# Performance work log

Measured on AMD Instinct MI355X. Metric: run time of the kernel, lower is better.

The kernel has to match this reference:

```python
import jax, jax.numpy as jnp
import numpy as np
from jax import lax

N, H, W, C = 4, 256, 256, 128
COUT = 128
BS_IN, BS_OUT, BSTR = 18, 16, 16  # gather block, conv-out block, block stride
N_ACTIVE = 512


def setup_inputs() -> dict:
    key = jax.random.key(0)
    ks = jax.random.split(key, 8)
    x = jax.random.normal(ks[0], (N, H, W, C), dtype=jnp.float32)
    w = jax.random.normal(ks[1], (3, 3, C, COUT), dtype=jnp.float32) * 0.05  # HWIO
    b = jax.random.normal(ks[2], (COUT,), dtype=jnp.float32) * 0.05
    gamma = jax.random.uniform(ks[3], (COUT,), dtype=jnp.float32, minval=0.5, maxval=1.5)
    beta = jax.random.normal(ks[4], (COUT,), dtype=jnp.float32) * 0.1
    mean = jax.random.normal(ks[5], (COUT,), dtype=jnp.float32) * 0.1
    var = jax.random.uniform(ks[6], (COUT,), dtype=jnp.float32, minval=0.5, maxval=1.5)
    # unique active block ids over the N x (H/16) x (W/16) grid -> disjoint scatter targets
    n_blocks = N * (H // BSTR) * (W // BSTR)
    active = jax.random.permutation(ks[7], n_blocks)[:N_ACTIVE].astype(jnp.int32)
    return {"x": x, "w": w, "b": b, "gamma": gamma, "beta": beta,
            "mean": mean, "var": var, "active": active}


def reference(x, w, b, gamma, beta, mean, var, active):
    n_, h_, w_, c_ = x.shape
    nby, nbx = h_ // BSTR, w_ // BSTR
    bn = active // (nby * nbx)
    rem = active % (nby * nbx)
    by = rem // nbx
    bx = rem % nbx

    # --- sparse_gather: overlapping BS_IN x BS_IN input blocks (zero-pad edges) ---
    pad = BS_IN - BS_OUT
    xp = jnp.pad(x, ((0, 0), (0, pad), (0, pad), (0, 0)))
    Hp, Wp = h_ + pad, w_ + pad
    d_in = jnp.arange(BS_IN, dtype=jnp.int32)
    hs = by[:, None] * BSTR + d_in[None, :]            # [Nb, 18]
    ws = bx[:, None] * BSTR + d_in[None, :]            # [Nb, 18]
    gidx = bn[:, None, None] * (Hp * Wp) + hs[:, :, None] * Wp + ws[:, None, :]
    p = xp.reshape(-1, c_)[gidx]                       # [Nb, 18, 18, C]

    # --- dense conv + BN(eval, eps=1e-3) + ReLU on gathered blocks ---
    q = lax.conv_general_dilated(p, w, window_strides=(1, 1), padding='VALID',
                                 dimension_numbers=('NHWC', 'HWIO', 'NHWC'))
    q = q + b
    q = (q - mean) * (gamma * lax.rsqrt(var + 1e-3)) + beta
    q = jax.nn.relu(q)                                 # [Nb, 16, 16, COUT]

    # --- sparse_scatter: write disjoint BS_OUT blocks back into a copy of x ---
    d_out = jnp.arange(BS_OUT, dtype=jnp.int32)
    hso = by[:, None] * BSTR + d_out[None, :]
    wso = bx[:, None] * BSTR + d_out[None, :]
    sidx = bn[:, None, None] * (h_ * w_) + hso[:, :, None] * w_ + wso[:, None, :]
    y = x.reshape(-1, c_).at[sidx.reshape(-1)].set(q.reshape(-1, q.shape[-1]))
    return y.reshape(n_, h_, w_, c_)
```

## Files before the change

### kernel.cpp

```cpp
#include <hip/hip_runtime.h>
#include <hip/hip_bf16.h>

#define H_ 256
#define W_ 256
#define C_ 128
#define NBPOS 1024
#define NACT 512

typedef __bf16 bf16x8 __attribute__((ext_vector_type(8)));
typedef float f32x4 __attribute__((ext_vector_type(4)));

#define SCALE_OFF 294912
#define SHIFT_OFF 295424
#define FLAGS_OFF 295936

__global__ void prep_w_kernel(const float* __restrict__ w, __bf16* __restrict__ wprep) {
  int o = blockIdx.x * 256 + threadIdx.x;
  int j = o & 7, cout = (o >> 3) & 127, k8 = (o >> 10) & 15, tap = o >> 14;
  wprep[o] = (__bf16)w[((size_t)tap * 128 + k8 * 8 + j) * 128 + cout];
}

__global__ void small_kernel(const float* __restrict__ b, const float* __restrict__ gamma,
                             const float* __restrict__ beta, const float* __restrict__ mean,
                             const float* __restrict__ var, const int* __restrict__ active,
                             float* __restrict__ scale, float* __restrict__ shift,
                             int* __restrict__ flags) {
  __shared__ unsigned mask[32];
  int tid = threadIdx.x;
  if (tid < 32) mask[tid] = 0u;
  __syncthreads();
  if (tid < NACT) {
    int a = active[tid];
    atomicOr(&mask[a >> 5], 1u << (a & 31));
  }
  if (tid < 128) {
    float s = gamma[tid] * rsqrtf(var[tid] + 1e-3f);
    scale[tid] = s;
    shift[tid] = (b[tid] - mean[tid]) * s + beta[tid];
  }
  __syncthreads();
  flags[tid] = (mask[tid >> 5] >> (tid & 31)) & 1u;
}

__global__ __launch_bounds__(256) void copy_kernel(const float* __restrict__ x,
                                                   const int* __restrict__ flags,
                                                   float* __restrict__ y) {
  int pb = blockIdx.x;
  if (flags[pb]) return;
  int bn = pb >> 8, by = (pb >> 4) & 15, bx = pb & 15;
  size_t base4 = ((((size_t)bn * H_ + by * 16) * W_ + bx * 16) * C_) >> 2;
  const f32x4* __restrict__ xs = (const f32x4*)x;
  f32x4* __restrict__ ys = (f32x4*)y;
#pragma unroll 4
  for (int i = 0; i < 32; ++i) {
    int lin = (i << 8) + threadIdx.x;
    int row = lin >> 9, rem = lin & 511;
    size_t idx4 = base4 + (size_t)row * (W_ * C_ / 4) + rem;
    f32x4 v = xs[idx4];
    __builtin_nontemporal_store(v, &ys[idx4]);
  }
}

__global__ __launch_bounds__(256, 4) void conv_kernel(
    const float* __restrict__ x, const __bf16* __restrict__ wprep,
    const float* __restrict__ scale, const float* __restrict__ shift,
    const int* __restrict__ active, float* __restrict__ y) {
  __shared__ unsigned char ldsA[180 * 128];
  __shared__ unsigned char ldsB[2][8192];

  const int tid = threadIdx.x;
  const int lane = tid & 63;
  const int wid = tid >> 6;
  const int aid = active[blockIdx.x >> 1];
  const int mh = blockIdx.x & 1;
  const int bn = aid >> 8, by = (aid >> 4) & 15, bx = aid & 15;
  const int h0 = by * 16, w0 = bx * 16;
  const int hm = h0 + mh * 8;
  const float* xb = x + (size_t)bn * (H_ * W_ * C_);

  f32x4 acc[2][8];
  f32x4 zero = {0.f, 0.f, 0.f, 0.f};
#pragma unroll
  for (int i = 0; i < 2; ++i)
#pragma unroll
    for (int j = 0; j < 8; ++j) acc[i][j] = zero;

  const uint4* wp4 = (const uint4*)wprep;
  uint4 t0, t1;
  auto load_t = [&](int u) {
    int ks = u % 18, h = u / 18;
    int tile = ((ks >> 1) << 2) + (h << 1) + (ks & 1);
    t0 = wp4[tile * 512 + tid];
    t1 = wp4[tile * 512 + 256 + tid];
  };
  auto stage = [&](int half) {
    for (int u = tid; u < 180 * 8; u += 256) {
      int s = u >> 3, c8 = u & 7;
      int pr = s / 18, col = s - pr * 18;
      int hs = hm + pr, wsp = w0 + col;
      float4 f0 = make_float4(0.f, 0.f, 0.f, 0.f), f1 = f0;
      if (hs < H_ && wsp < W_) {
        const float* p = xb + (size_t)(hs * W_ + wsp) * C_ + half * 64 + c8 * 8;
        f0 = *(const float4*)p;
        f1 = *(const float4*)(p + 4);
      }
      bf16x8 v;
      v[0] = (__bf16)f0.x; v[1] = (__bf16)f0.y; v[2] = (__bf16)f0.z; v[3] = (__bf16)f0.w;
      v[4] = (__bf16)f1.x; v[5] = (__bf16)f1.y; v[6] = (__bf16)f1.z; v[7] = (__bf16)f1.w;
      int lin = s * 128 + c8 * 16;
      *(bf16x8*)(&ldsA[lin ^ ((s & 7) << 4)]) = v;
    }
  };

  load_t(0);
  stage(0);
  ((uint4*)ldsB[0])[tid] = t0;
  ((uint4*)ldsB[0])[256 + tid] = t1;
  load_t(1);
  __syncthreads();

  const int koff = (lane >> 4) * 16;
  const int colb = (lane & 15) * 16;
  const int krow = (lane >> 4) * 2048;

  for (int u = 0; u < 36; ++u) {
    int cur = u & 1;
    if (u < 35) {
      ((uint4*)ldsB[cur ^ 1])[tid] = t0;
      ((uint4*)ldsB[cur ^ 1])[256 + tid] = t1;
      if (u < 34) load_t(u + 2);
    }
    int ks = u % 18;
    int tap = ks >> 1, kch = ks & 1;
    int dyv = tap / 3, dxv = tap - dyv * 3;

    bf16x8 a[2];
#pragma unroll
    for (int mi = 0; mi < 2; ++mi) {
      int srow = (wid * 2 + mi + dyv) * 18 + dxv + (lane & 15);
      int lin = srow * 128 + kch * 64 + koff;
      a[mi] = *(const bf16x8*)(&ldsA[lin ^ ((srow & 7) << 4)]);
    }
    bf16x8 bfr[8];
#pragma unroll
    for (int nb = 0; nb < 8; ++nb)
      bfr[nb] = *(const bf16x8*)(&ldsB[cur][krow + nb * 256 + colb]);
#pragma unroll
    for (int mi = 0; mi < 2; ++mi)
#pragma unroll
      for (int nb = 0; nb < 8; ++nb)
        acc[mi][nb] = __builtin_amdgcn_mfma_f32_16x16x32_bf16(a[mi], bfr[nb], acc[mi][nb], 0, 0, 0);

    __syncthreads();
    if (u == 17) {
      stage(1);
      __syncthreads();
    }
  }

  const int colc = lane & 15;
  float sc[8], sh[8];
#pragma unroll
  for (int nb = 0; nb < 8; ++nb) {
    sc[nb] = scale[nb * 16 + colc];
    sh[nb] = shift[nb * 16 + colc];
  }
  float* yb = y + (((size_t)bn * H_ + hm) * W_ + w0) * C_;
#pragma unroll
  for (int mi = 0; mi < 2; ++mi) {
    int oy = wid * 2 + mi;
#pragma unroll
    for (int r = 0; r < 4; ++r) {
      int ox = (lane >> 4) * 4 + r;
      float* yr = yb + ((size_t)oy * W_ + ox) * C_;
#pragma unroll
      for (int nb = 0; nb < 8; ++nb) {
        float v = acc[mi][nb][r] * sc[nb] + sh[nb];
        __builtin_nontemporal_store(fmaxf(v, 0.f), &yr[nb * 16 + colc]);
      }
    }
  }
}

extern "C" void kernel_launch(void* const* d_in, const int* in_sizes, int n_in,
                              void* d_out, int out_size, void* d_ws, size_t ws_size,
                              hipStream_t stream) {
  const float* x     = (const float*)d_in[0];
  const float* w     = (const float*)d_in[1];
  const float* b     = (const float*)d_in[2];
  const float* gamma = (const float*)d_in[3];
  const float* beta  = (const float*)d_in[4];
  const float* mean  = (const float*)d_in[5];
  const float* var   = (const float*)d_in[6];
  const int*   act   = (const int*)d_in[7];
  float* y = (float*)d_out;
  char* ws = (char*)d_ws;
  __bf16* wprep = (__bf16*)ws;
  float* scale = (float*)(ws + SCALE_OFF);
  float* shift = (float*)(ws + SHIFT_OFF);
  int* flags = (int*)(ws + FLAGS_OFF);

  prep_w_kernel<<<dim3(576), dim3(256), 0, stream>>>(w, wprep);
  small_kernel<<<dim3(1), dim3(1024), 0, stream>>>(b, gamma, beta, mean, var, act,
                                                   scale, shift, flags);
  copy_kernel<<<dim3(NBPOS), dim3(256), 0, stream>>>(x, flags, y);
  conv_kernel<<<dim3(NACT * 2), dim3(256), 0, stream>>>(x, wprep, scale, shift, act, y);
}
```

Baseline: 79.70 us.

## Merge prep kernels and interleave copy blocks with conv blocks in one launch

Folds the weight-prep and BN/flag kernels into one launch and compacts inactive block ids into a list, so no copy blocks are launched only to exit early. The copy of the inactive blocks is merged into the conv kernel, with every third workgroup doing a copy, so memory-bound copying overlaps with MFMA-bound conv work. This cuts two launches and the idle early-exit workgroups. In exchange the copy workgroups carry the conv kernel's LDS footprint and launch bounds, which may limit how many fit per CU.

Result: faster. 75.26 us (-5.6%).

```diff
diff --git a/kernel.cpp b/kernel.cpp
--- a/kernel.cpp
+++ b/kernel.cpp
@@ -12,25 +12,28 @@
 
 #define SCALE_OFF 294912
 #define SHIFT_OFF 295424
-#define FLAGS_OFF 295936
-
-__global__ void prep_w_kernel(const float* __restrict__ w, __bf16* __restrict__ wprep) {
-  int o = blockIdx.x * 256 + threadIdx.x;
-  int j = o & 7, cout = (o >> 3) & 127, k8 = (o >> 10) & 15, tap = o >> 14;
-  wprep[o] = (__bf16)w[((size_t)tap * 128 + k8 * 8 + j) * 128 + cout];
-}
-
-__global__ void small_kernel(const float* __restrict__ b, const float* __restrict__ gamma,
-                             const float* __restrict__ beta, const float* __restrict__ mean,
-                             const float* __restrict__ var, const int* __restrict__ active,
-                             float* __restrict__ scale, float* __restrict__ shift,
-                             int* __restrict__ flags) {
+#define INACT_OFF 295936
+
+__global__ void prep_kernel(const float* __restrict__ w, const float* __restrict__ b,
+                            const float* __restrict__ gamma, const float* __restrict__ beta,
+                            const float* __restrict__ mean, const float* __restrict__ var,
+                            const int* __restrict__ active,
+                            __bf16* __restrict__ wprep, float* __restrict__ scale,
+                            float* __restrict__ shift, int* __restrict__ inact) {
+  int blk = blockIdx.x, tid = threadIdx.x;
+  if (blk < 576) {
+    int o = blk * 256 + tid;
+    int j = o & 7, cout = (o >> 3) & 127, k8 = (o >> 10) & 15, tap = o >> 14;
+    wprep[o] = (__bf16)w[((size_t)tap * 128 + k8 * 8 + j) * 128 + cout];
+    return;
+  }
   __shared__ unsigned mask[32];
-  int tid = threadIdx.x;
+  __shared__ int cnt;
   if (tid < 32) mask[tid] = 0u;
+  if (tid == 0) cnt = 0;
   __syncthreads();
-  if (tid < NACT) {
-    int a = active[tid];
+  for (int i = tid; i < NACT; i += 256) {
+    int a = active[i];
     atomicOr(&mask[a >> 5], 1u << (a & 31));
   }
   if (tid < 128) {
@@ -39,40 +42,47 @@
     shift[tid] = (b[tid] - mean[tid]) * s + beta[tid];
   }
   __syncthreads();
-  flags[tid] = (mask[tid >> 5] >> (tid & 31)) & 1u;
+  for (int p = tid; p < NBPOS; p += 256) {
+    if (!((mask[p >> 5] >> (p & 31)) & 1u)) {
+      int q = atomicAdd(&cnt, 1);
+      inact[q] = p;
+    }
+  }
 }
 
-__global__ __launch_bounds__(256) void copy_kernel(const float* __restrict__ x,
-                                                   const int* __restrict__ flags,
-                                                   float* __restrict__ y) {
-  int pb = blockIdx.x;
-  if (flags[pb]) return;
-  int bn = pb >> 8, by = (pb >> 4) & 15, bx = pb & 15;
-  size_t base4 = ((((size_t)bn * H_ + by * 16) * W_ + bx * 16) * C_) >> 2;
-  const f32x4* __restrict__ xs = (const f32x4*)x;
-  f32x4* __restrict__ ys = (f32x4*)y;
-#pragma unroll 4
-  for (int i = 0; i < 32; ++i) {
-    int lin = (i << 8) + threadIdx.x;
-    int row = lin >> 9, rem = lin & 511;
-    size_t idx4 = base4 + (size_t)row * (W_ * C_ / 4) + rem;
-    f32x4 v = xs[idx4];
-    __builtin_nontemporal_store(v, &ys[idx4]);
-  }
-}
-
-__global__ __launch_bounds__(256, 4) void conv_kernel(
+__global__ __launch_bounds__(256, 4) void main_kernel(
     const float* __restrict__ x, const __bf16* __restrict__ wprep,
     const float* __restrict__ scale, const float* __restrict__ shift,
-    const int* __restrict__ active, float* __restrict__ y) {
+    const int* __restrict__ active, const int* __restrict__ inact,
+    float* __restrict__ y) {
   __shared__ unsigned char ldsA[180 * 128];
   __shared__ unsigned char ldsB[2][8192];
 
+  const int idx = blockIdx.x;
   const int tid = threadIdx.x;
+
+  if (idx % 3 == 2) {
+    const int cid = inact[idx / 3];
+    const int cn = cid >> 8, cy = (cid >> 4) & 15, cx = cid & 15;
+    const size_t base4 = ((((size_t)cn * H_ + cy * 16) * W_ + cx * 16) * C_) >> 2;
+    const f32x4* __restrict__ xs = (const f32x4*)x;
+    f32x4* __restrict__ ys = (f32x4*)y;
+#pragma unroll 4
+    for (int i = 0; i < 32; ++i) {
+      int lin = (i << 8) + tid;
+      int row = lin >> 9, rem = lin & 511;
+      size_t idx4 = base4 + (size_t)row * (W_ * C_ / 4) + rem;
+      f32x4 v = xs[idx4];
+      __builtin_nontemporal_store(v, &ys[idx4]);
+    }
+    return;
+  }
+
+  const int j = (idx / 3) * 2 + (idx % 3);
   const int lane = tid & 63;
   const int wid = tid >> 6;
-  const int aid = active[blockIdx.x >> 1];
-  const int mh = blockIdx.x & 1;
+  const int aid = active[j >> 1];
+  const int mh = j & 1;
   const int bn = aid >> 8, by = (aid >> 4) & 15, bx = aid & 15;
   const int h0 = by * 16, w0 = bx * 16;
   const int hm = h0 + mh * 8;
@@ -83,7 +93,7 @@
 #pragma unroll
   for (int i = 0; i < 2; ++i)
 #pragma unroll
-    for (int j = 0; j < 8; ++j) acc[i][j] = zero;
+    for (int jj = 0; jj < 8; ++jj) acc[i][jj] = zero;
 
   const uint4* wp4 = (const uint4*)wprep;
   uint4 t0, t1;
@@ -198,11 +208,9 @@
   __bf16* wprep = (__bf16*)ws;
   float* scale = (float*)(ws + SCALE_OFF);
   float* shift = (float*)(ws + SHIFT_OFF);
-  int* flags = (int*)(ws + FLAGS_OFF);
-
-  prep_w_kernel<<<dim3(576), dim3(256), 0, stream>>>(w, wprep);
-  small_kernel<<<dim3(1), dim3(1024), 0, stream>>>(b, gamma, beta, mean, var, act,
-                                                   scale, shift, flags);
-  copy_kernel<<<dim3(NBPOS), dim3(256), 0, stream>>>(x, flags, y);
-  conv_kernel<<<dim3(NACT * 2), dim3(256), 0, stream>>>(x, wprep, scale, shift, act, y);
+  int* inact = (int*)(ws + INACT_OFF);
+
+  prep_kernel<<<dim3(577), dim3(256), 0, stream>>>(w, b, gamma, beta, mean, var, act,
+                                                   wprep, scale, shift, inact);
+  main_kernel<<<dim3(1536), dim3(256), 0, stream>>>(x, wprep, scale, shift, act, inact, y);
 }
```
